# Kernel tuning notes

Measured on AMD Instinct MI355X. Metric: run time of the kernel, lower is better.

Reference implementation:

```python
import jax, jax.numpy as jnp
import numpy as np

N, B, D, K, H = 30000, 16, 32, 8, 8
DIST = 5.0
EPS = 1e-6


def setup_inputs() -> dict:
    key = jax.random.key(0)
    ks = jax.random.split(key, 16)
    sc = 1.0 / np.sqrt(D)
    inp = {
        'pos': jax.random.uniform(ks[0], (N, 3), jnp.float32) * 20.0,
        'node_features': jax.random.normal(ks[1], (N, D), jnp.float32),
        'batch': jnp.sort(jax.random.randint(ks[2], (N,), 0, B, dtype=jnp.int32)),
        'bessel_weights': jnp.linspace(jnp.pi, K * jnp.pi, K).astype(jnp.float32),
        'init_dummy': jax.random.normal(ks[3], (D,), jnp.float32),
        'Wq_dummy': jax.random.normal(ks[4], (D, D), jnp.float32) * sc,
        'Wq_graph': jax.random.normal(ks[5], (D, D), jnp.float32) * sc,
        'Wdot': jax.random.normal(ks[6], (D, D), jnp.float32) * sc,
        'W1_kd': jax.random.normal(ks[7], (K, H), jnp.float32) / np.sqrt(K),
        'W2_kd': jax.random.normal(ks[8], (H, D * D), jnp.float32) / np.sqrt(H),
        'W1_vd': jax.random.normal(ks[9], (K, H), jnp.float32) / np.sqrt(K),
        'W2_vd': jax.random.normal(ks[10], (H, D * D), jnp.float32) / np.sqrt(H),
        'W1_kg': jax.random.normal(ks[11], (K, H), jnp.float32) / np.sqrt(K),
        'W2_kg': jax.random.normal(ks[12], (H, D * D), jnp.float32) / np.sqrt(H),
        'W1_vg': jax.random.normal(ks[13], (K, H), jnp.float32) / np.sqrt(K),
        'W2_vg': jax.random.normal(ks[14], (H, D * D), jnp.float32) / np.sqrt(H),
    }
    return inp


def reference(pos, node_features, batch, bessel_weights, init_dummy,
              Wq_dummy, Wq_graph, Wdot,
              W1_kd, W2_kd, W1_vd, W2_vd, W1_kg, W2_kg, W1_vg, W2_vg):
    scale = 1.0 / np.sqrt(D)

    # --- dummy edge features: per-batch z extents + bessel basis ---
    z = pos[:, 2]                                            # [N]
    z_min = jax.ops.segment_min(z, batch, num_segments=B)    # [B]
    z_max = jax.ops.segment_max(z, batch, num_segments=B)    # [B]
    bot_len = z - z_min[batch] + DIST                        # [N]
    top_len = z_max[batch] + DIST - z                        # [N]

    def bessel(x):  # [N] -> [N,K]
        return jnp.sin(bessel_weights * x[:, None]) / (x[:, None] + EPS)

    edge = jnp.stack([bessel(bot_len), bessel(top_len)], axis=1)  # [N,2,K]

    # --- init dummy node features [B, 2, D] ---
    dummy = jnp.broadcast_to(init_dummy, (B, 2, D))

    def gen_w(W1, W2):  # conditional weight generator (silu MLP)
        return (jax.nn.silu(edge @ W1) @ W2).reshape(N, 2, D, D)

    # --- dummy nodes attend over graph nodes (segment softmax) ---
    wk = gen_w(W1_kd, W2_kd)                                 # [N,2,D,D]
    wv = gen_w(W1_vd, W2_vd)
    q = (dummy @ Wq_dummy)[batch]                            # [N,2,D]
    k = jnp.einsum('nd,nsde->nse', node_features, wk)        # [N,2,D]
    v = jnp.einsum('nd,nsde->nse', node_features, wv)
    s = jnp.einsum('nsq,qk,nsk->ns', q, Wdot, k) * scale     # [N,2]
    m = jax.ops.segment_max(s, batch, num_segments=B)
    e = jnp.exp(s - m[batch])
    zsum = jax.ops.segment_sum(e, batch, num_segments=B)
    attn = e / zsum[batch]                                   # [N,2]
    dummy_new = dummy + jax.ops.segment_sum(attn[..., None] * v, batch, num_segments=B)

    # --- graph nodes attend over (2) dummy nodes ---
    wkg = gen_w(W1_kg, W2_kg)
    wvg = gen_w(W1_vg, W2_vg)
    d_per = dummy_new[batch]                                 # [N,2,D]
    kg = jnp.einsum('nsd,nsde->nse', d_per, wkg)
    vg = jnp.einsum('nsd,nsde->nse', d_per, wvg)
    qg = node_features @ Wq_graph                            # [N,D]
    sg = jnp.einsum('nq,qk,nsk->ns', qg, Wdot, kg) * scale   # [N,2]
    ag = jax.nn.softmax(sg, axis=1)
    x_new = node_features + jnp.einsum('ns,nsd->nd', ag, vg)  # [N,D]
    return x_new
```

## Files before the change

### kernel.cpp

```cpp
#include <hip/hip_runtime.h>
#include <math.h>

#define NN 30000
#define BB 16
#define DD 32
#define KK 8
#define HH 8
#define DIST_C 5.0f
#define EPS_C 1e-6f
#define SCALE_C 0.17677669529663687f

#define WS_ZMIN 0
#define WS_ZMAX 16
#define WS_ZSUM 32
#define WS_QW   64
#define WS_PK   96
#define WS_WC   352
#define WS_T    1376
#define WS_AKG  9568
#define WS_AVG  17760

#define NPB 32

__device__ __forceinline__ unsigned fencode(float f) {
    unsigned u = __float_as_uint(f);
    return (u & 0x80000000u) ? ~u : (u | 0x80000000u);
}
__device__ __forceinline__ float fdecode(unsigned c) {
    return __uint_as_float((c & 0x80000000u) ? (c ^ 0x80000000u) : ~c);
}
__device__ __forceinline__ float silu(float x) { return x / (1.0f + expf(-x)); }

__device__ __forceinline__ void bessel_edges(float bw0, float x0, float x1, float edge[2][8]) {
    float xs[2]; xs[0] = x0; xs[1] = x1;
    #pragma unroll
    for (int s = 0; s < 2; ++s) {
        float x = xs[s];
        float inv = 1.0f / (x + EPS_C);
        float th = bw0 * x;
        float c2 = 2.0f * cosf(th);
        float skm1 = 0.0f;
        float sk = sinf(th);
        #pragma unroll
        for (int k = 0; k < 8; ++k) {
            edge[s][k] = sk * inv;
            float nx = c2 * sk - skm1;
            skm1 = sk;
            sk = nx;
        }
    }
}

__global__ __launch_bounds__(256) void k_init(const float* __restrict__ init_dummy,
                                              const float* __restrict__ Wq_dummy,
                                              const float* __restrict__ Wdot,
                                              const float* __restrict__ W2_kd,
                                              const float* __restrict__ Wq_graph,
                                              float* __restrict__ ws) {
    __shared__ float qvec[32];
    __shared__ float qWl[32];
    int t = threadIdx.x;
    unsigned* wsu = (unsigned*)ws;
    if (t < 16) { wsu[WS_ZMIN + t] = 0xFFFFFFFFu; wsu[WS_ZMAX + t] = 0u; }
    if (t < 32) ws[WS_ZSUM + t] = 0.0f;
    for (int i = t; i < 8192; i += 256) ws[WS_T + i] = 0.0f;
    if (t < 32) {
        float acc = 0.0f;
        for (int d = 0; d < 32; ++d) acc += init_dummy[d] * Wq_dummy[d * 32 + t];
        qvec[t] = acc;
    }
    __syncthreads();
    if (t < 32) {
        float acc = 0.0f;
        for (int e = 0; e < 32; ++e) acc += qvec[e] * Wdot[e * 32 + t];
        qWl[t] = acc;
        ws[WS_QW + t] = acc;
    }
    __syncthreads();
    {
        int h = t >> 5, d = t & 31;
        float acc = 0.0f;
        for (int e = 0; e < 32; ++e) acc += W2_kd[h * 1024 + d * 32 + e] * qWl[e];
        ws[WS_PK + t] = acc;
    }
    for (int i = t; i < 1024; i += 256) {
        int d = i >> 5, e = i & 31;
        float acc = 0.0f;
        for (int m = 0; m < 32; ++m) acc += Wq_graph[d * 32 + m] * Wdot[m * 32 + e];
        ws[WS_WC + i] = acc;
    }
}

__global__ __launch_bounds__(256) void k_zminmax(const float* __restrict__ pos,
                                                 const int* __restrict__ batch,
                                                 float* __restrict__ ws) {
    __shared__ unsigned zl[16], zh[16];
    int t = threadIdx.x;
    if (t < 16) { zl[t] = 0xFFFFFFFFu; zh[t] = 0u; }
    __syncthreads();
    int n = blockIdx.x * 256 + t;
    if (n < NN) {
        unsigned c = fencode(pos[3 * n + 2]);
        int b = batch[n];
        atomicMin(&zl[b], c);
        atomicMax(&zh[b], c);
    }
    __syncthreads();
    unsigned* wsu = (unsigned*)ws;
    if (t < 16) {
        if (zl[t] != 0xFFFFFFFFu) atomicMin(&wsu[WS_ZMIN + t], zl[t]);
        if (zh[t] != 0u)          atomicMax(&wsu[WS_ZMAX + t], zh[t]);
    }
}

__global__ __launch_bounds__(256) void k_phase1(const float* __restrict__ pos,
                                                const int* __restrict__ batch,
                                                const float* __restrict__ nf,
                                                const float* __restrict__ bw,
                                                const float* __restrict__ W1_kd,
                                                const float* __restrict__ W1_vd,
                                                float* __restrict__ ws) {
    __shared__ __align__(16) float Fl[NPB * 36];
    __shared__ float Lw[NPB * 17];
    __shared__ int   Lb[NPB];
    __shared__ __align__(16) float Pk[256];
    __shared__ float W1kd[64], W1vd[64], zsl[32];
    int t = threadIdx.x;
    if (t < 64) { W1kd[t] = W1_kd[t]; W1vd[t] = W1_vd[t]; }
    Pk[t] = ws[WS_PK + t];
    if (t < 32) zsl[t] = 0.0f;

    int li = t >> 3, g = t & 7;
    int n0 = blockIdx.x * NPB;
    int n = n0 + li;
    bool valid = n < NN;
    float4 fv4 = make_float4(0.f, 0.f, 0.f, 0.f);
    int b = 0;
    if (valid) {
        b = batch[n];
        fv4 = ((const float4*)nf)[n * 8 + g];
        ((float4*)(Fl + li * 36))[g] = fv4;
        if (g == 0) Lb[li] = b;
    } else {
        if (g == 0) Lb[li] = -1;
    }
    __syncthreads();

    if (valid) {
        const unsigned* wsu = (const unsigned*)ws;
        float z = pos[3 * n + 2];
        float zmin = fdecode(wsu[WS_ZMIN + b]);
        float zmax = fdecode(wsu[WS_ZMAX + b]);
        float edge[2][8];
        bessel_edges(bw[0], z - zmin + DIST_C, zmax + DIST_C - z, edge);

        float up[8];
        const float4* Pk4 = (const float4*)Pk;
        #pragma unroll
        for (int h = 0; h < 8; ++h) {
            float4 p = Pk4[h * 8 + g];
            up[h] = fv4.x * p.x + fv4.y * p.y + fv4.z * p.z + fv4.w * p.w;
        }
        float kd0, kd1;
        {
            float p0 = 0.f, p1 = 0.f;
            #pragma unroll
            for (int k = 0; k < 8; ++k) {
                float w = W1kd[k * 8 + g];
                p0 += edge[0][k] * w;
                p1 += edge[1][k] * w;
            }
            kd0 = silu(p0); kd1 = silu(p1);
        }
        int lanebase = (t & 63) & 56;
        float sp0 = 0.f, sp1 = 0.f;
        #pragma unroll
        for (int h = 0; h < 8; ++h) {
            float a0 = __shfl(kd0, lanebase + h, 64);
            float a1 = __shfl(kd1, lanebase + h, 64);
            sp0 += a0 * up[h];
            sp1 += a1 * up[h];
        }
        #pragma unroll
        for (int m = 1; m < 8; m <<= 1) {
            sp0 += __shfl_xor(sp0, m, 64);
            sp1 += __shfl_xor(sp1, m, 64);
        }
        float ev0 = expf(sp0 * SCALE_C);
        float ev1 = expf(sp1 * SCALE_C);
        if (g == 0) {
            atomicAdd(&zsl[b * 2 + 0], ev0);
            atomicAdd(&zsl[b * 2 + 1], ev1);
        }
        float q0 = 0.f, q1 = 0.f;
        #pragma unroll
        for (int k = 0; k < 8; ++k) {
            float w = W1vd[k * 8 + g];
            q0 += edge[0][k] * w;
            q1 += edge[1][k] * w;
        }
        Lw[li * 17 + g]     = ev0 * silu(q0);
        Lw[li * 17 + 8 + g] = ev1 * silu(q1);
    }
    __syncthreads();
    if (t < 32 && zsl[t] != 0.0f) atomicAdd(&ws[WS_ZSUM + t], zsl[t]);

    int count = NN - n0; if (count > NPB) count = NPB;
    int bf = Lb[0], bl = Lb[count - 1];
    int sh = t & 15, dp = t >> 4;
    for (int b2 = bf; b2 <= bl; ++b2) {
        float a0 = 0.f, a1 = 0.f;
        for (int i = 0; i < count; ++i) {
            if (Lb[i] != b2) continue;
            float w = Lw[i * 17 + sh];
            float2 x = *(const float2*)(Fl + i * 36 + 2 * dp);
            a0 += w * x.x;
            a1 += w * x.y;
        }
        float* Tb = ws + WS_T + b2 * 512 + sh * 32 + 2 * dp;
        atomicAdd(&Tb[0], a0);
        atomicAdd(&Tb[1], a1);
    }
}

__global__ __launch_bounds__(256) void k_batch(const float* __restrict__ init_dummy,
                                               const float* __restrict__ W2_vd,
                                               const float* __restrict__ W2_kg,
                                               const float* __restrict__ W2_vg,
                                               float* __restrict__ ws) {
    int bs = blockIdx.x;
    int b = bs >> 1, s = bs & 1;
    int t = threadIdx.x;
    __shared__ float Tl[256];
    __shared__ float part[256];
    __shared__ float dn[32];
    Tl[t] = ws[WS_T + b * 512 + s * 256 + t];
    __syncthreads();
    {
        int h = t >> 5, e = t & 31;
        float acc = 0.0f;
        #pragma unroll
        for (int d = 0; d < 32; ++d) acc += Tl[h * 32 + d] * W2_vd[h * 1024 + d * 32 + e];
        part[t] = acc;
    }
    __syncthreads();
    if (t < 32) {
        float acc = 0.0f;
        #pragma unroll
        for (int h = 0; h < 8; ++h) acc += part[h * 32 + t];
        float zs = ws[WS_ZSUM + b * 2 + s];
        dn[t] = init_dummy[t] + acc / zs;
    }
    __syncthreads();
    {
        int h = t >> 5, e = t & 31;
        float ak = 0.0f, av = 0.0f;
        #pragma unroll
        for (int d = 0; d < 32; ++d) {
            float dv = dn[d];
            ak += dv * W2_kg[h * 1024 + d * 32 + e];
            av += dv * W2_vg[h * 1024 + d * 32 + e];
        }
        ws[WS_AKG + b * 512 + s * 256 + t] = ak;
        ws[WS_AVG + b * 512 + s * 256 + t] = av;
    }
}

__global__ __launch_bounds__(256) void k_final(const float* __restrict__ pos,
                                               const int* __restrict__ batch,
                                               const float* __restrict__ nf,
                                               const float* __restrict__ bw,
                                               const float* __restrict__ W1_kg,
                                               const float* __restrict__ W1_vg,
                                               const float* __restrict__ ws,
                                               float* __restrict__ out) {
    __shared__ __align__(16) float Wc[1024];
    __shared__ __align__(16) float Fl[NPB * 36];
    __shared__ float W1kg[64], W1vg[64];
    int t = threadIdx.x;
    for (int i = t; i < 1024; i += 256) Wc[i] = ws[WS_WC + i];
    if (t < 64) { W1kg[t] = W1_kg[t]; W1vg[t] = W1_vg[t]; }

    int li = t >> 3, g = t & 7;
    int n0 = blockIdx.x * NPB;
    int n = n0 + li;
    bool valid = n < NN;
    float4 fv4 = make_float4(0.f, 0.f, 0.f, 0.f);
    if (valid) {
        fv4 = ((const float4*)nf)[n * 8 + g];
        ((float4*)(Fl + li * 36))[g] = fv4;
    }
    __syncthreads();
    if (!valid) return;

    int b = batch[n];
    const unsigned* wsu = (const unsigned*)ws;
    float z = pos[3 * n + 2];
    float zmin = fdecode(wsu[WS_ZMIN + b]);
    float zmax = fdecode(wsu[WS_ZMAX + b]);
    float edge[2][8];
    bessel_edges(bw[0], z - zmin + DIST_C, zmax + DIST_C - z, edge);

    float ak0, ak1, av0, av1;
    {
        float pk0 = 0.f, pk1 = 0.f, pv0 = 0.f, pv1 = 0.f;
        #pragma unroll
        for (int k = 0; k < 8; ++k) {
            float wk = W1kg[k * 8 + g];
            float wv = W1vg[k * 8 + g];
            pk0 += edge[0][k] * wk; pk1 += edge[1][k] * wk;
            pv0 += edge[0][k] * wv; pv1 += edge[1][k] * wv;
        }
        ak0 = silu(pk0); ak1 = silu(pk1);
        av0 = silu(pv0); av1 = silu(pv1);
    }

    float f[32];
    {
        const float4* myF4 = (const float4*)(Fl + li * 36);
        #pragma unroll
        for (int j = 0; j < 8; ++j) {
            float4 v = myF4[j];
            f[4 * j] = v.x; f[4 * j + 1] = v.y; f[4 * j + 2] = v.z; f[4 * j + 3] = v.w;
        }
    }
    float4 q4 = make_float4(0.f, 0.f, 0.f, 0.f);
    const float4* Wc4 = (const float4*)Wc;
    #pragma unroll
    for (int d = 0; d < 32; ++d) {
        float fd = f[d];
        float4 w = Wc4[d * 8 + g];
        q4.x += fd * w.x; q4.y += fd * w.y; q4.z += fd * w.z; q4.w += fd * w.w;
    }

    int lanebase = (t & 63) & 56;
    const float4* Ak4 = (const float4*)(ws + WS_AKG);
    const float4* Av4 = (const float4*)(ws + WS_AVG);
    float p0 = 0.f, p1 = 0.f;
    #pragma unroll
    for (int h = 0; h < 8; ++h) {
        float4 a0 = Ak4[b * 128 + h * 8 + g];
        float4 a1 = Ak4[b * 128 + 64 + h * 8 + g];
        float d0 = q4.x * a0.x + q4.y * a0.y + q4.z * a0.z + q4.w * a0.w;
        float d1 = q4.x * a1.x + q4.y * a1.y + q4.z * a1.z + q4.w * a1.w;
        p0 += __shfl(ak0, lanebase + h, 64) * d0;
        p1 += __shfl(ak1, lanebase + h, 64) * d1;
    }
    #pragma unroll
    for (int m = 1; m < 8; m <<= 1) {
        p0 += __shfl_xor(p0, m, 64);
        p1 += __shfl_xor(p1, m, 64);
    }
    float sg0 = p0 * SCALE_C, sg1 = p1 * SCALE_C;
    float mm = fmaxf(sg0, sg1);
    float e0 = expf(sg0 - mm), e1 = expf(sg1 - mm);
    float inv = 1.0f / (e0 + e1);
    float ag0 = e0 * inv, ag1 = e1 * inv;

    float4 x4 = fv4;
    #pragma unroll
    for (int h = 0; h < 8; ++h) {
        float w0 = ag0 * __shfl(av0, lanebase + h, 64);
        float w1 = ag1 * __shfl(av1, lanebase + h, 64);
        float4 a0 = Av4[b * 128 + h * 8 + g];
        float4 a1 = Av4[b * 128 + 64 + h * 8 + g];
        x4.x += w0 * a0.x + w1 * a1.x;
        x4.y += w0 * a0.y + w1 * a1.y;
        x4.z += w0 * a0.z + w1 * a1.z;
        x4.w += w0 * a0.w + w1 * a1.w;
    }
    ((float4*)out)[n * 8 + g] = x4;
}

extern "C" void kernel_launch(void* const* d_in, const int* in_sizes, int n_in,
                              void* d_out, int out_size, void* d_ws, size_t ws_size,
                              hipStream_t stream) {
    const float* pos        = (const float*)d_in[0];
    const float* nf         = (const float*)d_in[1];
    const int*   batch      = (const int*)d_in[2];
    const float* bw         = (const float*)d_in[3];
    const float* init_dummy = (const float*)d_in[4];
    const float* Wq_dummy   = (const float*)d_in[5];
    const float* Wq_graph   = (const float*)d_in[6];
    const float* Wdot       = (const float*)d_in[7];
    const float* W1_kd      = (const float*)d_in[8];
    const float* W2_kd      = (const float*)d_in[9];
    const float* W1_vd      = (const float*)d_in[10];
    const float* W2_vd      = (const float*)d_in[11];
    const float* W1_kg      = (const float*)d_in[12];
    const float* W2_kg      = (const float*)d_in[13];
    const float* W1_vg      = (const float*)d_in[14];
    const float* W2_vg      = (const float*)d_in[15];
    float* ws  = (float*)d_ws;
    float* out = (float*)d_out;

    int nblk1 = (NN + 255) / 256;
    int nblk8 = (NN + NPB - 1) / NPB;
    hipLaunchKernelGGL(k_init, dim3(1), dim3(256), 0, stream,
                       init_dummy, Wq_dummy, Wdot, W2_kd, Wq_graph, ws);
    hipLaunchKernelGGL(k_zminmax, dim3(nblk1), dim3(256), 0, stream, pos, batch, ws);
    hipLaunchKernelGGL(k_phase1, dim3(nblk8), dim3(256), 0, stream,
                       pos, batch, nf, bw, W1_kd, W1_vd, ws);
    hipLaunchKernelGGL(k_batch, dim3(32), dim3(256), 0, stream,
                       init_dummy, W2_vd, W2_kg, W2_vg, ws);
    hipLaunchKernelGGL(k_final, dim3(nblk8), dim3(256), 0, stream,
                       pos, batch, nf, bw, W1_kg, W1_vg, ws, out);
}
```

Before: 124.3 us.

## Merge init and z-extent kernels, fold per-batch dummy update into final kernel

Replaces the separate init and atomic z-min/max kernels with one multi-role pre kernel. Its first 16 blocks binary-search the sorted batch array and reduce z extents per segment with wave shuffles, while the other blocks do the weight precompute and workspace zeroing. The per-batch dummy-update kernel is removed. Each final block instead recomputes the dummy key/value projections for the (at most two) batches its 32 nodes span, in shared memory. This cuts two launches and the global atomics but repeats the W2 projections in every one of about 938 blocks. It also assumes no 32-node block spans more than two batches.

```diff
diff --git a/kernel.cpp b/kernel.cpp
--- a/kernel.cpp
+++ b/kernel.cpp
@@ -2,10 +2,6 @@
 #include <math.h>
 
 #define NN 30000
-#define BB 16
-#define DD 32
-#define KK 8
-#define HH 8
 #define DIST_C 5.0f
 #define EPS_C 1e-6f
 #define SCALE_C 0.17677669529663687f
@@ -13,27 +9,15 @@
 #define WS_ZMIN 0
 #define WS_ZMAX 16
 #define WS_ZSUM 32
-#define WS_QW   64
-#define WS_PK   96
-#define WS_WC   352
-#define WS_T    1376
-#define WS_AKG  9568
-#define WS_AVG  17760
-
-#define NPB 32
-
-__device__ __forceinline__ unsigned fencode(float f) {
-    unsigned u = __float_as_uint(f);
-    return (u & 0x80000000u) ? ~u : (u | 0x80000000u);
-}
-__device__ __forceinline__ float fdecode(unsigned c) {
-    return __uint_as_float((c & 0x80000000u) ? (c ^ 0x80000000u) : ~c);
-}
+#define WS_T    64
+#define WS_PK   8256
+#define WS_WC   8512
+
 __device__ __forceinline__ float silu(float x) { return x / (1.0f + expf(-x)); }
 
 __device__ __forceinline__ void bessel_edges(float bw0, float x0, float x1, float edge[2][8]) {
     float xs[2]; xs[0] = x0; xs[1] = x1;
-    #pragma unroll
+#pragma unroll
     for (int s = 0; s < 2; ++s) {
         float x = xs[s];
         float inv = 1.0f / (x + EPS_C);
@@ -41,75 +25,81 @@
         float c2 = 2.0f * cosf(th);
         float skm1 = 0.0f;
         float sk = sinf(th);
-        #pragma unroll
+#pragma unroll
         for (int k = 0; k < 8; ++k) {
             edge[s][k] = sk * inv;
             float nx = c2 * sk - skm1;
-            skm1 = sk;
-            sk = nx;
+            skm1 = sk; sk = nx;
         }
     }
 }
 
-__global__ __launch_bounds__(256) void k_init(const float* __restrict__ init_dummy,
-                                              const float* __restrict__ Wq_dummy,
-                                              const float* __restrict__ Wdot,
-                                              const float* __restrict__ W2_kd,
-                                              const float* __restrict__ Wq_graph,
-                                              float* __restrict__ ws) {
-    __shared__ float qvec[32];
-    __shared__ float qWl[32];
-    int t = threadIdx.x;
-    unsigned* wsu = (unsigned*)ws;
-    if (t < 16) { wsu[WS_ZMIN + t] = 0xFFFFFFFFu; wsu[WS_ZMAX + t] = 0u; }
-    if (t < 32) ws[WS_ZSUM + t] = 0.0f;
-    for (int i = t; i < 8192; i += 256) ws[WS_T + i] = 0.0f;
-    if (t < 32) {
-        float acc = 0.0f;
-        for (int d = 0; d < 32; ++d) acc += init_dummy[d] * Wq_dummy[d * 32 + t];
-        qvec[t] = acc;
-    }
-    __syncthreads();
-    if (t < 32) {
-        float acc = 0.0f;
-        for (int e = 0; e < 32; ++e) acc += qvec[e] * Wdot[e * 32 + t];
-        qWl[t] = acc;
-        ws[WS_QW + t] = acc;
-    }
-    __syncthreads();
-    {
+__global__ __launch_bounds__(256) void k_pre(const float* __restrict__ pos,
+                                             const int* __restrict__ batch,
+                                             const float* __restrict__ init_dummy,
+                                             const float* __restrict__ Wq_dummy,
+                                             const float* __restrict__ Wdot,
+                                             const float* __restrict__ W2_kd,
+                                             const float* __restrict__ Wq_graph,
+                                             float* __restrict__ ws) {
+    int t = threadIdx.x, blk = blockIdx.x;
+    if (blk < 16) {
+        __shared__ int bnd2[2];
+        __shared__ float r[8];
+        if (t < 2) {
+            int target = blk + t;
+            int lo = 0, hi = NN;
+            while (lo < hi) { int mid = (lo + hi) >> 1; if (batch[mid] < target) lo = mid + 1; else hi = mid; }
+            bnd2[t] = lo;
+        }
+        __syncthreads();
+        int s0 = bnd2[0], s1 = bnd2[1];
+        float zmn = 3.4e38f, zmx = -3.4e38f;
+        for (int i = s0 + t; i < s1; i += 256) {
+            float v = pos[3 * i + 2];
+            zmn = fminf(zmn, v); zmx = fmaxf(zmx, v);
+        }
+#pragma unroll
+        for (int off = 1; off < 64; off <<= 1) {
+            zmn = fminf(zmn, __shfl_xor(zmn, off, 64));
+            zmx = fmaxf(zmx, __shfl_xor(zmx, off, 64));
+        }
+        if ((t & 63) == 0) { r[(t >> 6) * 2] = zmn; r[(t >> 6) * 2 + 1] = zmx; }
+        __syncthreads();
+        if (t == 0) {
+            ws[WS_ZMIN + blk] = fminf(fminf(r[0], r[2]), fminf(r[4], r[6]));
+            ws[WS_ZMAX + blk] = fmaxf(fmaxf(r[1], r[3]), fmaxf(r[5], r[7]));
+        }
+    } else if (blk == 16) {
+        __shared__ float qv[32], qW[32];
+        if (t < 32) {
+            float acc = 0.f;
+            for (int d = 0; d < 32; ++d) acc += init_dummy[d] * Wq_dummy[d * 32 + t];
+            qv[t] = acc;
+        }
+        __syncthreads();
+        if (t < 32) {
+            float acc = 0.f;
+            for (int e = 0; e < 32; ++e) acc += qv[e] * Wdot[e * 32 + t];
+            qW[t] = acc;
+        }
+        __syncthreads();
         int h = t >> 5, d = t & 31;
-        float acc = 0.0f;
-        for (int e = 0; e < 32; ++e) acc += W2_kd[h * 1024 + d * 32 + e] * qWl[e];
+        float acc = 0.f;
+        for (int e = 0; e < 32; ++e) acc += W2_kd[h * 1024 + d * 32 + e] * qW[e];
         ws[WS_PK + t] = acc;
-    }
-    for (int i = t; i < 1024; i += 256) {
-        int d = i >> 5, e = i & 31;
-        float acc = 0.0f;
-        for (int m = 0; m < 32; ++m) acc += Wq_graph[d * 32 + m] * Wdot[m * 32 + e];
-        ws[WS_WC + i] = acc;
-    }
-}
-
-__global__ __launch_bounds__(256) void k_zminmax(const float* __restrict__ pos,
-                                                 const int* __restrict__ batch,
-                                                 float* __restrict__ ws) {
-    __shared__ unsigned zl[16], zh[16];
-    int t = threadIdx.x;
-    if (t < 16) { zl[t] = 0xFFFFFFFFu; zh[t] = 0u; }
-    __syncthreads();
-    int n = blockIdx.x * 256 + t;
-    if (n < NN) {
-        unsigned c = fencode(pos[3 * n + 2]);
-        int b = batch[n];
-        atomicMin(&zl[b], c);
-        atomicMax(&zh[b], c);
-    }
-    __syncthreads();
-    unsigned* wsu = (unsigned*)ws;
-    if (t < 16) {
-        if (zl[t] != 0xFFFFFFFFu) atomicMin(&wsu[WS_ZMIN + t], zl[t]);
-        if (zh[t] != 0u)          atomicMax(&wsu[WS_ZMAX + t], zh[t]);
+    } else if (blk == 17) {
+        for (int i = t; i < 1024; i += 256) {
+            int d = i >> 5, e = i & 31;
+            float acc = 0.f;
+            for (int m = 0; m < 32; ++m) acc += Wq_graph[d * 32 + m] * Wdot[m * 32 + e];
+            ws[WS_WC + i] = acc;
+        }
+    } else {
+        int idx = blk - 18;
+        ws[WS_T + idx * 512 + t] = 0.f;
+        ws[WS_T + idx * 512 + 256 + t] = 0.f;
+        if (idx == 0 && t < 32) ws[WS_ZSUM + t] = 0.f;
     }
 }
 
@@ -120,18 +110,18 @@
                                                 const float* __restrict__ W1_kd,
                                                 const float* __restrict__ W1_vd,
                                                 float* __restrict__ ws) {
-    __shared__ __align__(16) float Fl[NPB * 36];
-    __shared__ float Lw[NPB * 17];
-    __shared__ int   Lb[NPB];
+    __shared__ __align__(16) float Fl[32 * 36];
+    __shared__ float Lw[32 * 17];
+    __shared__ int   Lb[32];
     __shared__ __align__(16) float Pk[256];
     __shared__ float W1kd[64], W1vd[64], zsl[32];
     int t = threadIdx.x;
     if (t < 64) { W1kd[t] = W1_kd[t]; W1vd[t] = W1_vd[t]; }
     Pk[t] = ws[WS_PK + t];
-    if (t < 32) zsl[t] = 0.0f;
+    if (t < 32) zsl[t] = 0.f;
 
     int li = t >> 3, g = t & 7;
-    int n0 = blockIdx.x * NPB;
+    int n0 = blockIdx.x * 32;
     int n = n0 + li;
     bool valid = n < NN;
     float4 fv4 = make_float4(0.f, 0.f, 0.f, 0.f);
@@ -147,16 +137,15 @@
     __syncthreads();
 
     if (valid) {
-        const unsigned* wsu = (const unsigned*)ws;
         float z = pos[3 * n + 2];
-        float zmin = fdecode(wsu[WS_ZMIN + b]);
-        float zmax = fdecode(wsu[WS_ZMAX + b]);
+        float zminb = ws[WS_ZMIN + b];
+        float zmaxb = ws[WS_ZMAX + b];
         float edge[2][8];
-        bessel_edges(bw[0], z - zmin + DIST_C, zmax + DIST_C - z, edge);
+        bessel_edges(bw[0], z - zminb + DIST_C, zmaxb + DIST_C - z, edge);
 
         float up[8];
         const float4* Pk4 = (const float4*)Pk;
-        #pragma unroll
+#pragma unroll
         for (int h = 0; h < 8; ++h) {
             float4 p = Pk4[h * 8 + g];
             up[h] = fv4.x * p.x + fv4.y * p.y + fv4.z * p.z + fv4.w * p.w;
@@ -164,7 +153,7 @@
         float kd0, kd1;
         {
             float p0 = 0.f, p1 = 0.f;
-            #pragma unroll
+#pragma unroll
             for (int k = 0; k < 8; ++k) {
                 float w = W1kd[k * 8 + g];
                 p0 += edge[0][k] * w;
@@ -174,14 +163,12 @@
         }
         int lanebase = (t & 63) & 56;
         float sp0 = 0.f, sp1 = 0.f;
-        #pragma unroll
+#pragma unroll
         for (int h = 0; h < 8; ++h) {
-            float a0 = __shfl(kd0, lanebase + h, 64);
-            float a1 = __shfl(kd1, lanebase + h, 64);
-            sp0 += a0 * up[h];
-            sp1 += a1 * up[h];
-        }
-        #pragma unroll
+            sp0 += __shfl(kd0, lanebase + h, 64) * up[h];
+            sp1 += __shfl(kd1, lanebase + h, 64) * up[h];
+        }
+#pragma unroll
         for (int m = 1; m < 8; m <<= 1) {
             sp0 += __shfl_xor(sp0, m, 64);
             sp1 += __shfl_xor(sp1, m, 64);
@@ -193,7 +180,7 @@
             atomicAdd(&zsl[b * 2 + 1], ev1);
         }
         float q0 = 0.f, q1 = 0.f;
-        #pragma unroll
+#pragma unroll
         for (int k = 0; k < 8; ++k) {
             float w = W1vd[k * 8 + g];
             q0 += edge[0][k] * w;
@@ -203,9 +190,9 @@
         Lw[li * 17 + 8 + g] = ev1 * silu(q1);
     }
     __syncthreads();
-    if (t < 32 && zsl[t] != 0.0f) atomicAdd(&ws[WS_ZSUM + t], zsl[t]);
-
-    int count = NN - n0; if (count > NPB) count = NPB;
+    if (t < 32 && zsl[t] != 0.f) atomicAdd(&ws[WS_ZSUM + t], zsl[t]);
+
+    int count = NN - n0; if (count > 32) count = 32;
     int bf = Lb[0], bl = Lb[count - 1];
     int sh = t & 15, dp = t >> 4;
     for (int b2 = bf; b2 <= bl; ++b2) {
@@ -223,147 +210,160 @@
     }
 }
 
-__global__ __launch_bounds__(256) void k_batch(const float* __restrict__ init_dummy,
-                                               const float* __restrict__ W2_vd,
-                                               const float* __restrict__ W2_kg,
-                                               const float* __restrict__ W2_vg,
-                                               float* __restrict__ ws) {
-    int bs = blockIdx.x;
-    int b = bs >> 1, s = bs & 1;
+__global__ __launch_bounds__(256) void k_fin(const float* __restrict__ pos,
+                                             const int* __restrict__ batch,
+                                             const float* __restrict__ nf,
+                                             const float* __restrict__ bw,
+                                             const float* __restrict__ W1_kg,
+                                             const float* __restrict__ W1_vg,
+                                             const float* __restrict__ init_dummy,
+                                             const float* __restrict__ W2_vd,
+                                             const float* __restrict__ W2_kg,
+                                             const float* __restrict__ W2_vg,
+                                             const float* __restrict__ ws,
+                                             float* __restrict__ out) {
+    __shared__ __align__(16) float Wc[1024];
+    __shared__ __align__(16) float Fl[32 * 36];
+    __shared__ int   Lb[32];
+    __shared__ float W1kg[64], W1vg[64];
+    __shared__ float Tl[2][512];
+    __shared__ float part[2][512];
+    __shared__ float dn[2][64];
+    __shared__ __align__(16) float AK[2][512], AV[2][512];
+
     int t = threadIdx.x;
-    __shared__ float Tl[256];
-    __shared__ float part[256];
-    __shared__ float dn[32];
-    Tl[t] = ws[WS_T + b * 512 + s * 256 + t];
+    int li = t >> 3, g = t & 7;
+    int lanebase = (t & 63) & 56;
+    for (int i = t; i < 1024; i += 256) Wc[i] = ws[WS_WC + i];
+    if (t < 64) { W1kg[t] = W1_kg[t]; W1vg[t] = W1_vg[t]; }
+
+    int n0 = blockIdx.x * 32;
+    int n = n0 + li;
+    int count = NN - n0; if (count > 32) count = 32;
+    bool valid = li < count;
+    float4 fv4 = make_float4(0.f, 0.f, 0.f, 0.f);
+    float z = 0.f;
+    int b = 0;
+    if (valid) {
+        b = batch[n];
+        fv4 = ((const float4*)nf)[n * 8 + g];
+        ((float4*)(Fl + li * 36))[g] = fv4;
+        z = pos[3 * n + 2];
+        if (g == 0) Lb[li] = b;
+    }
+    __syncthreads();
+    int bf = Lb[0], bl = Lb[count - 1];
+
+    Tl[0][t]       = ws[WS_T + bf * 512 + t];
+    Tl[0][256 + t] = ws[WS_T + bf * 512 + 256 + t];
+    Tl[1][t]       = ws[WS_T + bl * 512 + t];
+    Tl[1][256 + t] = ws[WS_T + bl * 512 + 256 + t];
     __syncthreads();
     {
         int h = t >> 5, e = t & 31;
-        float acc = 0.0f;
-        #pragma unroll
-        for (int d = 0; d < 32; ++d) acc += Tl[h * 32 + d] * W2_vd[h * 1024 + d * 32 + e];
-        part[t] = acc;
-    }
-    __syncthreads();
-    if (t < 32) {
-        float acc = 0.0f;
-        #pragma unroll
-        for (int h = 0; h < 8; ++h) acc += part[h * 32 + t];
-        float zs = ws[WS_ZSUM + b * 2 + s];
-        dn[t] = init_dummy[t] + acc / zs;
+        float a00 = 0.f, a01 = 0.f, a10 = 0.f, a11 = 0.f;
+        for (int d = 0; d < 32; ++d) {
+            float w2 = W2_vd[h * 1024 + d * 32 + e];
+            a00 += Tl[0][h * 32 + d] * w2;
+            a01 += Tl[0][256 + h * 32 + d] * w2;
+            a10 += Tl[1][h * 32 + d] * w2;
+            a11 += Tl[1][256 + h * 32 + d] * w2;
+        }
+        part[0][t] = a00; part[0][256 + t] = a01;
+        part[1][t] = a10; part[1][256 + t] = a11;
+    }
+    __syncthreads();
+    if (t < 64) {
+        int s = t >> 5, dd = t & 31;
+        float acc0 = 0.f, acc1 = 0.f;
+        for (int h = 0; h < 8; ++h) {
+            acc0 += part[0][s * 256 + h * 32 + dd];
+            acc1 += part[1][s * 256 + h * 32 + dd];
+        }
+        float id = init_dummy[dd];
+        dn[0][t] = id + acc0 / ws[WS_ZSUM + bf * 2 + s];
+        dn[1][t] = id + acc1 / ws[WS_ZSUM + bl * 2 + s];
     }
     __syncthreads();
     {
         int h = t >> 5, e = t & 31;
-        float ak = 0.0f, av = 0.0f;
-        #pragma unroll
+        float k00 = 0.f, k01 = 0.f, k10 = 0.f, k11 = 0.f;
+        float v00 = 0.f, v01 = 0.f, v10 = 0.f, v11 = 0.f;
         for (int d = 0; d < 32; ++d) {
-            float dv = dn[d];
-            ak += dv * W2_kg[h * 1024 + d * 32 + e];
-            av += dv * W2_vg[h * 1024 + d * 32 + e];
-        }
-        ws[WS_AKG + b * 512 + s * 256 + t] = ak;
-        ws[WS_AVG + b * 512 + s * 256 + t] = av;
-    }
-}
-
-__global__ __launch_bounds__(256) void k_final(const float* __restrict__ pos,
-                                               const int* __restrict__ batch,
-                                               const float* __restrict__ nf,
-                                               const float* __restrict__ bw,
-                                               const float* __restrict__ W1_kg,
-                                               const float* __restrict__ W1_vg,
-                                               const float* __restrict__ ws,
-                                               float* __restrict__ out) {
-    __shared__ __align__(16) float Wc[1024];
-    __shared__ __align__(16) float Fl[NPB * 36];
-    __shared__ float W1kg[64], W1vg[64];
-    int t = threadIdx.x;
-    for (int i = t; i < 1024; i += 256) Wc[i] = ws[WS_WC + i];
-    if (t < 64) { W1kg[t] = W1_kg[t]; W1vg[t] = W1_vg[t]; }
-
-    int li = t >> 3, g = t & 7;
-    int n0 = blockIdx.x * NPB;
-    int n = n0 + li;
-    bool valid = n < NN;
-    float4 fv4 = make_float4(0.f, 0.f, 0.f, 0.f);
-    if (valid) {
-        fv4 = ((const float4*)nf)[n * 8 + g];
-        ((float4*)(Fl + li * 36))[g] = fv4;
-    }
-    __syncthreads();
+            float w2k = W2_kg[h * 1024 + d * 32 + e];
+            float w2v = W2_vg[h * 1024 + d * 32 + e];
+            k00 += dn[0][d] * w2k;      v00 += dn[0][d] * w2v;
+            k01 += dn[0][32 + d] * w2k; v01 += dn[0][32 + d] * w2v;
+            k10 += dn[1][d] * w2k;      v10 += dn[1][d] * w2v;
+            k11 += dn[1][32 + d] * w2k; v11 += dn[1][32 + d] * w2v;
+        }
+        AK[0][t] = k00; AK[0][256 + t] = k01;
+        AK[1][t] = k10; AK[1][256 + t] = k11;
+        AV[0][t] = v00; AV[0][256 + t] = v01;
+        AV[1][t] = v10; AV[1][256 + t] = v11;
+    }
+    __syncthreads();
+
     if (!valid) return;
-
-    int b = batch[n];
-    const unsigned* wsu = (const unsigned*)ws;
-    float z = pos[3 * n + 2];
-    float zmin = fdecode(wsu[WS_ZMIN + b]);
-    float zmax = fdecode(wsu[WS_ZMAX + b]);
+    int slot = (b == bf) ? 0 : 1;
+    const float4* Ak4 = (const float4*)AK[slot];
+    const float4* Av4 = (const float4*)AV[slot];
+    const float4* Wc4 = (const float4*)Wc;
+
+    float zminb = ws[WS_ZMIN + b];
+    float zmaxb = ws[WS_ZMAX + b];
     float edge[2][8];
-    bessel_edges(bw[0], z - zmin + DIST_C, zmax + DIST_C - z, edge);
-
-    float ak0, ak1, av0, av1;
+    bessel_edges(bw[0], z - zminb + DIST_C, zmaxb + DIST_C - z, edge);
+
+    float sk0, sk1, sv0, sv1;
     {
         float pk0 = 0.f, pk1 = 0.f, pv0 = 0.f, pv1 = 0.f;
-        #pragma unroll
+#pragma unroll
         for (int k = 0; k < 8; ++k) {
             float wk = W1kg[k * 8 + g];
             float wv = W1vg[k * 8 + g];
             pk0 += edge[0][k] * wk; pk1 += edge[1][k] * wk;
             pv0 += edge[0][k] * wv; pv1 += edge[1][k] * wv;
         }
-        ak0 = silu(pk0); ak1 = silu(pk1);
-        av0 = silu(pv0); av1 = silu(pv1);
-    }
-
-    float f[32];
-    {
-        const float4* myF4 = (const float4*)(Fl + li * 36);
-        #pragma unroll
-        for (int j = 0; j < 8; ++j) {
-            float4 v = myF4[j];
-            f[4 * j] = v.x; f[4 * j + 1] = v.y; f[4 * j + 2] = v.z; f[4 * j + 3] = v.w;
-        }
+        sk0 = silu(pk0); sk1 = silu(pk1);
+        sv0 = silu(pv0); sv1 = silu(pv1);
     }
     float4 q4 = make_float4(0.f, 0.f, 0.f, 0.f);
-    const float4* Wc4 = (const float4*)Wc;
-    #pragma unroll
+    const float* myF = Fl + li * 36;
+#pragma unroll
     for (int d = 0; d < 32; ++d) {
-        float fd = f[d];
+        float fd = myF[d];
         float4 w = Wc4[d * 8 + g];
         q4.x += fd * w.x; q4.y += fd * w.y; q4.z += fd * w.z; q4.w += fd * w.w;
     }
-
-    int lanebase = (t & 63) & 56;
-    const float4* Ak4 = (const float4*)(ws + WS_AKG);
-    const float4* Av4 = (const float4*)(ws + WS_AVG);
     float p0 = 0.f, p1 = 0.f;
-    #pragma unroll
+#pragma unroll
     for (int h = 0; h < 8; ++h) {
-        float4 a0 = Ak4[b * 128 + h * 8 + g];
-        float4 a1 = Ak4[b * 128 + 64 + h * 8 + g];
+        float4 a0 = Ak4[h * 8 + g];
+        float4 a1 = Ak4[64 + h * 8 + g];
         float d0 = q4.x * a0.x + q4.y * a0.y + q4.z * a0.z + q4.w * a0.w;
         float d1 = q4.x * a1.x + q4.y * a1.y + q4.z * a1.z + q4.w * a1.w;
-        p0 += __shfl(ak0, lanebase + h, 64) * d0;
-        p1 += __shfl(ak1, lanebase + h, 64) * d1;
-    }
-    #pragma unroll
+        p0 += __shfl(sk0, lanebase + h, 64) * d0;
+        p1 += __shfl(sk1, lanebase + h, 64) * d1;
+    }
+#pragma unroll
     for (int m = 1; m < 8; m <<= 1) {
         p0 += __shfl_xor(p0, m, 64);
         p1 += __shfl_xor(p1, m, 64);
     }
     float sg0 = p0 * SCALE_C, sg1 = p1 * SCALE_C;
-    float mm = fmaxf(sg0, sg1);
-    float e0 = expf(sg0 - mm), e1 = expf(sg1 - mm);
+    float mx = fmaxf(sg0, sg1);
+    float e0 = expf(sg0 - mx), e1 = expf(sg1 - mx);
     float inv = 1.0f / (e0 + e1);
     float ag0 = e0 * inv, ag1 = e1 * inv;
 
     float4 x4 = fv4;
-    #pragma unroll
+#pragma unroll
     for (int h = 0; h < 8; ++h) {
-        float w0 = ag0 * __shfl(av0, lanebase + h, 64);
-        float w1 = ag1 * __shfl(av1, lanebase + h, 64);
-        float4 a0 = Av4[b * 128 + h * 8 + g];
-        float4 a1 = Av4[b * 128 + 64 + h * 8 + g];
+        float w0 = ag0 * __shfl(sv0, lanebase + h, 64);
+        float w1 = ag1 * __shfl(sv1, lanebase + h, 64);
+        float4 a0 = Av4[h * 8 + g];
+        float4 a1 = Av4[64 + h * 8 + g];
         x4.x += w0 * a0.x + w1 * a1.x;
         x4.y += w0 * a0.y + w1 * a1.y;
         x4.z += w0 * a0.z + w1 * a1.z;
@@ -394,15 +394,12 @@
     float* ws  = (float*)d_ws;
     float* out = (float*)d_out;
 
-    int nblk1 = (NN + 255) / 256;
-    int nblk8 = (NN + NPB - 1) / NPB;
-    hipLaunchKernelGGL(k_init, dim3(1), dim3(256), 0, stream,
-                       init_dummy, Wq_dummy, Wdot, W2_kd, Wq_graph, ws);
-    hipLaunchKernelGGL(k_zminmax, dim3(nblk1), dim3(256), 0, stream, pos, batch, ws);
-    hipLaunchKernelGGL(k_phase1, dim3(nblk8), dim3(256), 0, stream,
+    int nblk = (NN + 31) / 32;
+    hipLaunchKernelGGL(k_pre, dim3(34), dim3(256), 0, stream,
+                       pos, batch, init_dummy, Wq_dummy, Wdot, W2_kd, Wq_graph, ws);
+    hipLaunchKernelGGL(k_phase1, dim3(nblk), dim3(256), 0, stream,
                        pos, batch, nf, bw, W1_kd, W1_vd, ws);
-    hipLaunchKernelGGL(k_batch, dim3(32), dim3(256), 0, stream,
-                       init_dummy, W2_vd, W2_kg, W2_vg, ws);
-    hipLaunchKernelGGL(k_final, dim3(nblk8), dim3(256), 0, stream,
-                       pos, batch, nf, bw, W1_kg, W1_vg, ws, out);
+    hipLaunchKernelGGL(k_fin, dim3(nblk), dim3(256), 0, stream,
+                       pos, batch, nf, bw, W1_kg, W1_vg, init_dummy,
+                       W2_vd, W2_kg, W2_vg, ws, out);
 }
```

New measurement: 124.0 us. No clear change (-0.3%).
